# Optimization experiments

Measured on AMD Instinct MI355X. Metric: run time of the kernel, lower is better.

## Reference

```python
import jax, jax.numpy as jnp
import numpy as np

B, L, D = 4, 4096, 1024
H = 16
DK = D // H  # 64
EPS = 1e-5


def setup_inputs() -> dict:
    key = jax.random.key(0)
    ks = jax.random.split(key, 9)
    s = 1.0 / np.sqrt(D)
    return {
        "Q": jax.random.normal(ks[0], (B, L, D), dtype=jnp.float32),
        "W_Q": jax.random.uniform(ks[1], (D, D), jnp.float32, -s, s),
        "b_Q": jax.random.uniform(ks[2], (D,), jnp.float32, -s, s),
        "W_K": jax.random.uniform(ks[3], (D, D), jnp.float32, -s, s),
        "b_K": jax.random.uniform(ks[4], (D,), jnp.float32, -s, s),
        "W_V": jax.random.uniform(ks[5], (D, D), jnp.float32, -s, s),
        "b_V": jax.random.uniform(ks[6], (D,), jnp.float32, -s, s),
        "W_O": jax.random.uniform(ks[7], (D, D), jnp.float32, -s, s),
        "b_O": jax.random.uniform(ks[8], (D,), jnp.float32, -s, s),
    }


def reference(Q, W_Q, b_Q, W_K, b_K, W_V, b_V, W_O, b_O):
    # Projections (torch Linear: x @ W.T + b). K = V = Q (self-attention).
    q = (Q @ W_Q.T + b_Q).reshape(B, L, H, DK)  # blhd
    k = (Q @ W_K.T + b_K).reshape(B, L, H, DK)
    v = (Q @ W_V.T + b_V).reshape(B, L, H, DK)

    phi_q = jax.nn.elu(q) + 1.0
    phi_k = jax.nn.elu(k) + 1.0

    # KV outer-product accumulation over sequence: [b,h,d,m]
    KV = jnp.einsum('blhd,blhm->bhdm', phi_k, v)
    K_sum = phi_k.sum(axis=1)                       # [b,h,d]
    Z = 1.0 / (jnp.einsum('blhd,bhd->blh', phi_q, K_sum) + EPS)
    V_new = jnp.einsum('blhd,bhdm->blhm', phi_q, KV) * Z[..., None]

    out = V_new.reshape(B, L, H * DK) @ W_O.T + b_O  # [b,L,d_model]
    return out
```

## Files before the change

### kernel.cpp

```cpp
#include <hip/hip_runtime.h>

typedef unsigned short u16;
typedef unsigned int   u32;
typedef __attribute__((ext_vector_type(8))) short short8;
typedef __attribute__((ext_vector_type(4))) float f32x4;
typedef __attribute__((ext_vector_type(4))) u16   u16x4;

#define NB 4
#define SL 4096
#define DM 1024
#define NH 16
#define DK 64

__device__ __forceinline__ u16 f2bf(float f) {
  u32 u = __builtin_bit_cast(u32, f);
  u = (u + 0x7fffu + ((u >> 16) & 1u)) >> 16;
  return (u16)u;
}
__device__ __forceinline__ float bf2f(u16 v) {
  u32 u = ((u32)v) << 16;
  return __builtin_bit_cast(float, u);
}
__device__ __forceinline__ float eluP1(float x) {
  return x > 0.f ? x + 1.f : __expf(x);
}
__device__ __forceinline__ void gll16(const u16* g, u16* l) {
  __builtin_amdgcn_global_load_lds((const __attribute__((address_space(1))) void*)g,
                                   (__attribute__((address_space(3))) void*)l, 16, 0, 0);
}

__global__ void cvt_f32_bf16(const float* __restrict__ in, u16* __restrict__ out, int n4) {
  int i = blockIdx.x * 256 + threadIdx.x;
  if (i < n4) {
    f32x4 f = *(const f32x4*)(in + (size_t)i * 4);
    u16x4 o = { f2bf(f[0]), f2bf(f[1]), f2bf(f[2]), f2bf(f[3]) };
    *(u16x4*)(out + (size_t)i * 4) = o;
  }
}

__global__ void cvt_w(const float* __restrict__ WQ, const float* __restrict__ WK,
                      const float* __restrict__ WV, const float* __restrict__ WO,
                      u16* __restrict__ Wqkv, u16* __restrict__ Wobf) {
  int r = blockIdx.x >> 10;
  int i = (blockIdx.x & 1023) * 256 + threadIdx.x;
  const float* src = r == 0 ? WQ : r == 1 ? WK : r == 2 ? WV : WO;
  u16* dst = (r == 3) ? Wobf : Wqkv + (size_t)r * 1048576;
  f32x4 f = *(const f32x4*)(src + (size_t)i * 4);
  u16x4 o = { f2bf(f[0]), f2bf(f[1]), f2bf(f[2]), f2bf(f[3]) };
  *(u16x4*)(dst + (size_t)i * 4) = o;
}

__global__ void pack_bias(const float* __restrict__ bQ, const float* __restrict__ bK,
                          const float* __restrict__ bV, float* __restrict__ biasQKV) {
  int i = blockIdx.x * 256 + threadIdx.x;
  float v = (i < 1024) ? bQ[i] : (i < 2048) ? bK[i - 1024] : bV[i - 2048];
  biasQKV[i] = v;
}

__global__ __launch_bounds__(256) void gemm_qkv(const u16* __restrict__ A,
                                                const u16* __restrict__ Wqkv,
                                                const float* __restrict__ biasQKV,
                                                u16* __restrict__ phiq,
                                                u16* __restrict__ phiKT,
                                                u16* __restrict__ vT) {
  const int K = 1024;
  const int bId = blockIdx.x;
  const int xcd = bId & 7, s = bId >> 3;
  const int tile_n = s >> 4;
  const int tile_m = xcd * 16 + (s & 15);
  const int region = tile_n >> 3;

  const int tid = threadIdx.x, lane = tid & 63, wv = tid >> 6;
  const int i16 = lane & 15, q = lane >> 4;
  const int waveR = wv >> 1, waveC = wv & 1;

  __shared__ u16 smem[17408];

  const int rbase = wv * 32 + (lane >> 2);
  const int kc = (lane & 3) ^ ((rbase >> 1) & 3);
  const u16* Ag = A + (size_t)(tile_m * 128 + rbase) * K + kc * 8;
  const u16* Wg = Wqkv + (size_t)(tile_n * 128 + rbase) * K + kc * 8;

  f32x4 acc[4][4] = {};

  {
    u16* XsB = smem + wv * 1024;
    u16* WsB = smem + 4096 + wv * 1024;
    gll16(Ag, XsB);
    gll16(Ag + 16 * K, XsB + 512);
    gll16(Wg, WsB);
    gll16(Wg + 16 * K, WsB + 512);
  }

  for (int k = 0; k < 32; k++) {
    const int cur = k & 1;
    __syncthreads();
    if (k < 31) {
      const int nxt = cur ^ 1;
      const int k0 = (k + 1) * 32;
      u16* XsB = smem + nxt * 8192 + wv * 1024;
      u16* WsB = smem + nxt * 8192 + 4096 + wv * 1024;
      gll16(Ag + k0,          XsB);
      gll16(Ag + k0 + 16 * K, XsB + 512);
      gll16(Wg + k0,          WsB);
      gll16(Wg + k0 + 16 * K, WsB + 512);
    }
    const u16* Xc = smem + cur * 8192;
    const u16* Wc = Xc + 4096;
    const u16* aT = (region == 0) ? Wc : Xc;
    const u16* bT = (region == 0) ? Xc : Wc;

    short8 af[4], bfr[4];
#pragma unroll
    for (int t = 0; t < 4; t++) {
      int m = waveR * 64 + t * 16 + i16;
      af[t] = *(const short8*)(aT + m * 32 + ((q ^ ((m >> 1) & 3)) << 3));
    }
#pragma unroll
    for (int u = 0; u < 4; u++) {
      int m = waveC * 64 + u * 16 + i16;
      bfr[u] = *(const short8*)(bT + m * 32 + ((q ^ ((m >> 1) & 3)) << 3));
    }
#pragma unroll
    for (int t = 0; t < 4; t++)
#pragma unroll
      for (int u = 0; u < 4; u++)
        acc[t][u] = __builtin_amdgcn_mfma_f32_16x16x32_bf16(af[t], bfr[u], acc[t][u], 0, 0, 0);
  }

  __syncthreads();
  u16* T = smem;
#pragma unroll
  for (int t = 0; t < 4; t++) {
#pragma unroll
    for (int u = 0; u < 4; u++) {
      int cI = waveC * 64 + u * 16 + i16;
      int rI = waveR * 64 + t * 16 + q * 4;
      u16x4 o;
      if (region == 0) {
        f32x4 b4 = *(const f32x4*)(biasQKV + tile_n * 128 + rI);
#pragma unroll
        for (int r = 0; r < 4; r++) o[r] = f2bf(eluP1(acc[t][u][r] + b4[r]));
      } else {
        float bs = biasQKV[tile_n * 128 + cI];
#pragma unroll
        for (int r = 0; r < 4; r++) {
          float vv = acc[t][u][r] + bs;
          if (region == 1) vv = eluP1(vv);
          o[r] = f2bf(vv);
        }
      }
      *(u16x4*)(T + cI * 136 + rI) = o;
    }
  }
  __syncthreads();
  {
    const int Rl = tid >> 4, j = tid & 15;
    u16* dst = (region == 1) ? phiKT : vT;
#pragma unroll
    for (int p = 0; p < 8; p++) {
      int R = p * 16 + Rl;
      short8 v8 = *(const short8*)(T + R * 136 + j * 8);
      if (region == 0) {
        *(short8*)(phiq + (size_t)(tile_m * 128 + R) * DM + tile_n * 128 + j * 8) = v8;
      } else {
        int n_loc = tile_n * 128 + R - region * 1024;
        int bI = tile_m >> 5;
        int l = (tile_m & 31) * 128 + j * 8;
        *(short8*)(dst + ((size_t)bI * 1024 + n_loc) * 4096 + l) = v8;
      }
    }
  }
}

__global__ __launch_bounds__(256) void gemm_out(const u16* __restrict__ A,
                                                const u16* __restrict__ W,
                                                const float* __restrict__ bias,
                                                float* __restrict__ outp) {
  const int K = 1024;
  const int bId = blockIdx.x;
  const int xcd = bId & 7, s = bId >> 3;
  const int tile_n = s >> 4;
  const int tile_m = xcd * 16 + (s & 15);

  const int tid = threadIdx.x, lane = tid & 63, wv = tid >> 6;
  const int i16 = lane & 15, q = lane >> 4;
  const int waveR = wv >> 1, waveC = wv & 1;

  __shared__ u16 smem[17408];

  const int rbase = wv * 32 + (lane >> 2);
  const int kc = (lane & 3) ^ ((rbase >> 1) & 3);
  const u16* Ag = A + (size_t)(tile_m * 128 + rbase) * K + kc * 8;
  const u16* Wg = W + (size_t)(tile_n * 128 + rbase) * K + kc * 8;

  f32x4 acc[4][4] = {};

  {
    u16* XsB = smem + wv * 1024;
    u16* WsB = smem + 4096 + wv * 1024;
    gll16(Ag, XsB);
    gll16(Ag + 16 * K, XsB + 512);
    gll16(Wg, WsB);
    gll16(Wg + 16 * K, WsB + 512);
  }

  for (int k = 0; k < 32; k++) {
    const int cur = k & 1;
    __syncthreads();
    if (k < 31) {
      const int nxt = cur ^ 1;
      const int k0 = (k + 1) * 32;
      u16* XsB = smem + nxt * 8192 + wv * 1024;
      u16* WsB = smem + nxt * 8192 + 4096 + wv * 1024;
      gll16(Ag + k0,          XsB);
      gll16(Ag + k0 + 16 * K, XsB + 512);
      gll16(Wg + k0,          WsB);
      gll16(Wg + k0 + 16 * K, WsB + 512);
    }
    const u16* Xc = smem + cur * 8192;
    const u16* Wc = Xc + 4096;

    short8 af[4], bfr[4];
#pragma unroll
    for (int t = 0; t < 4; t++) {
      int m = waveR * 64 + t * 16 + i16;
      af[t] = *(const short8*)(Wc + m * 32 + ((q ^ ((m >> 1) & 3)) << 3));
    }
#pragma unroll
    for (int u = 0; u < 4; u++) {
      int m = waveC * 64 + u * 16 + i16;
      bfr[u] = *(const short8*)(Xc + m * 32 + ((q ^ ((m >> 1) & 3)) << 3));
    }
#pragma unroll
    for (int t = 0; t < 4; t++)
#pragma unroll
      for (int u = 0; u < 4; u++)
        acc[t][u] = __builtin_amdgcn_mfma_f32_16x16x32_bf16(af[t], bfr[u], acc[t][u], 0, 0, 0);
  }

  float* Tf = (float*)smem;
#pragma unroll
  for (int half = 0; half < 2; half++) {
    __syncthreads();
    if (waveR == half) {
#pragma unroll
      for (int t = 0; t < 4; t++) {
#pragma unroll
        for (int u = 0; u < 4; u++) {
          int cI = waveC * 64 + u * 16 + i16;
          int rIh = t * 16 + q * 4;
          f32x4 b4 = *(const f32x4*)(bias + tile_n * 128 + half * 64 + rIh);
          f32x4 o;
#pragma unroll
          for (int r = 0; r < 4; r++) o[r] = acc[t][u][r] + b4[r];
          *(f32x4*)(Tf + cI * 68 + rIh) = o;
        }
      }
    }
    __syncthreads();
    const int Rl = tid >> 4, j = tid & 15;
#pragma unroll
    for (int p = 0; p < 8; p++) {
      int R = p * 16 + Rl;
      f32x4 v = *(const f32x4*)(Tf + R * 68 + j * 4);
      *(f32x4*)(outp + (size_t)(tile_m * 128 + R) * DM + tile_n * 128 + half * 64 + j * 4) = v;
    }
  }
}

__global__ __launch_bounds__(256) void kv_partial(const u16* __restrict__ phiKT,
                                                  const u16* __restrict__ vT,
                                                  float* __restrict__ part,
                                                  float* __restrict__ ksumP) {
  int bh = blockIdx.x >> 2, chunk = blockIdx.x & 3;
  int tid = threadIdx.x, lane = tid & 63, wv = tid >> 6;
  int i16 = lane & 15, q = lane >> 4;
  const u16* Ab = phiKT + (size_t)bh * DK * SL;
  const u16* Bb = vT + (size_t)bh * DK * SL;
  int l0 = (chunk * 4 + wv) * 256;
  f32x4 acc[4][4] = {};
  float ks[4] = {};
  for (int kk = 0; kk < 256; kk += 32) {
    int col = l0 + kk + q * 8;
    short8 af[4], bfr[4];
#pragma unroll
    for (int t = 0; t < 4; t++) af[t] = *(const short8*)(Ab + (size_t)(t * 16 + i16) * SL + col);
#pragma unroll
    for (int u = 0; u < 4; u++) bfr[u] = *(const short8*)(Bb + (size_t)(u * 16 + i16) * SL + col);
#pragma unroll
    for (int t = 0; t < 4; t++)
#pragma unroll
      for (int j = 0; j < 8; j++) ks[t] += bf2f((u16)af[t][j]);
#pragma unroll
    for (int t = 0; t < 4; t++)
#pragma unroll
      for (int u = 0; u < 4; u++)
        acc[t][u] = __builtin_amdgcn_mfma_f32_16x16x32_bf16(af[t], bfr[u], acc[t][u], 0, 0, 0);
  }
  __shared__ float red[4][64][64];
  __shared__ float ksl[4][4][64];
#pragma unroll
  for (int t = 0; t < 4; t++)
#pragma unroll
    for (int u = 0; u < 4; u++)
#pragma unroll
      for (int r = 0; r < 4; r++)
        red[wv][t * 16 + q * 4 + r][u * 16 + i16] = acc[t][u][r];
#pragma unroll
  for (int t = 0; t < 4; t++) ksl[wv][q][t * 16 + i16] = ks[t];
  __syncthreads();
  int d = tid >> 2, mg = (tid & 3) * 16;
#pragma unroll
  for (int c = 0; c < 4; c++) {
    int m = mg + c * 4;
    f32x4 o;
#pragma unroll
    for (int r = 0; r < 4; r++)
      o[r] = red[0][d][m + r] + red[1][d][m + r] + red[2][d][m + r] + red[3][d][m + r];
    *(f32x4*)(part + ((size_t)(chunk * 64 + bh) * 64 + d) * 64 + m) = o;
  }
  if (tid < 64) {
    float s = 0.f;
#pragma unroll
    for (int w2 = 0; w2 < 4; w2++)
#pragma unroll
      for (int q2 = 0; q2 < 4; q2++) s += ksl[w2][q2][tid];
    ksumP[chunk * 4096 + bh * 64 + tid] = s;
  }
}

__global__ __launch_bounds__(256) void kv_finalize(const float* __restrict__ part,
                                                   const float* __restrict__ ksumP,
                                                   u16* __restrict__ KVt,
                                                   float* __restrict__ Ksum) {
  int bh = blockIdx.x, tid = threadIdx.x;
  for (int e = tid; e < 4096; e += 256) {
    int d = e >> 6, m = e & 63;
    float s = part[((size_t)(0 * 64 + bh) * 64 + d) * 64 + m]
            + part[((size_t)(1 * 64 + bh) * 64 + d) * 64 + m]
            + part[((size_t)(2 * 64 + bh) * 64 + d) * 64 + m]
            + part[((size_t)(3 * 64 + bh) * 64 + d) * 64 + m];
    KVt[(size_t)bh * 4096 + m * 64 + d] = f2bf(s);
  }
  if (tid < 64) {
    float s = ksumP[0 * 4096 + bh * 64 + tid] + ksumP[1 * 4096 + bh * 64 + tid]
            + ksumP[2 * 4096 + bh * 64 + tid] + ksumP[3 * 4096 + bh * 64 + tid];
    Ksum[bh * 64 + tid] = s;
  }
}

__global__ __launch_bounds__(256) void vnew_kernel(const u16* __restrict__ phiq,
                                                   const u16* __restrict__ KVt,
                                                   const float* __restrict__ Ksum,
                                                   u16* __restrict__ Vnew) {
  int bh = blockIdx.x >> 5, lt = blockIdx.x & 31;
  int b = bh >> 4, h = bh & 15;
  int tid = threadIdx.x, lane = tid & 63, wv = tid >> 6;
  int i16 = lane & 15, q = lane >> 4;
  int waveM = wv & 1, waveL = wv >> 1;

  __shared__ float Zs[128];
  __shared__ float Pp[128][2];
  __shared__ u16 T[128 * 72];
  {
    int l = tid >> 1, half = tid & 1;
    const u16* pr = phiq + (size_t)(b * SL + lt * 128 + l) * DM + h * 64 + half * 32;
    float s = 0.f;
    for (int i = 0; i < 32; i += 8) {
      short8 v8 = *(const short8*)(pr + i);
#pragma unroll
      for (int j = 0; j < 8; j++) s += bf2f((u16)v8[j]) * Ksum[bh * 64 + half * 32 + i + j];
    }
    Pp[l][half] = s;
  }
  __syncthreads();
  if (tid < 128) Zs[tid] = 1.0f / (Pp[tid][0] + Pp[tid][1] + 1e-5f);
  __syncthreads();

  f32x4 acc[2][4] = {};
#pragma unroll
  for (int step = 0; step < 2; step++) {
    int d0 = step * 32 + q * 8;
    short8 af[2], bfr[4];
#pragma unroll
    for (int t = 0; t < 2; t++) {
      int m = waveM * 32 + t * 16 + i16;
      af[t] = *(const short8*)(KVt + (size_t)bh * 4096 + m * 64 + d0);
    }
#pragma unroll
    for (int u = 0; u < 4; u++) {
      int l = lt * 128 + waveL * 64 + u * 16 + i16;
      bfr[u] = *(const short8*)(phiq + (size_t)(b * SL + l) * DM + h * 64 + d0);
    }
#pragma unroll
    for (int t = 0; t < 2; t++)
#pragma unroll
      for (int u = 0; u < 4; u++)
        acc[t][u] = __builtin_amdgcn_mfma_f32_16x16x32_bf16(af[t], bfr[u], acc[t][u], 0, 0, 0);
  }

#pragma unroll
  for (int t = 0; t < 2; t++) {
#pragma unroll
    for (int u = 0; u < 4; u++) {
      int cI = waveL * 64 + u * 16 + i16;
      int nI = waveM * 32 + t * 16 + q * 4;
      float z = Zs[cI];
      u16x4 o;
#pragma unroll
      for (int r = 0; r < 4; r++) o[r] = f2bf(acc[t][u][r] * z);
      *(u16x4*)(T + cI * 72 + nI) = o;
    }
  }
  __syncthreads();
  {
    const int Rl = tid >> 3, j = tid & 7;
#pragma unroll
    for (int p = 0; p < 4; p++) {
      int R = p * 32 + Rl;
      short8 v8 = *(const short8*)(T + R * 72 + j * 8);
      *(short8*)(Vnew + (size_t)(b * SL + lt * 128 + R) * DM + h * 64 + j * 8) = v8;
    }
  }
}

extern "C" void kernel_launch(void* const* d_in, const int* in_sizes, int n_in,
                              void* d_out, int out_size, void* d_ws, size_t ws_size,
                              hipStream_t stream) {
  const float* Qf = (const float*)d_in[0];
  const float* WQ = (const float*)d_in[1];
  const float* bQ = (const float*)d_in[2];
  const float* WK = (const float*)d_in[3];
  const float* bK = (const float*)d_in[4];
  const float* WV = (const float*)d_in[5];
  const float* bV = (const float*)d_in[6];
  const float* WO = (const float*)d_in[7];
  const float* bO = (const float*)d_in[8];

  const size_t MB = 1024ull * 1024ull;
  char* ws = (char*)d_ws;
  u16* Qbf     = (u16*)(ws + 0);
  u16* Vnew    = (u16*)(ws + 0);
  u16* Wqkv    = (u16*)(ws + 32 * MB);
  u16* Wobf    = (u16*)(ws + 38 * MB);
  float* biasQKV = (float*)(ws + 40 * MB);
  u16* phiq    = (u16*)(ws + 41 * MB);
  u16* phiKT   = (u16*)(ws + 73 * MB);
  u16* vT      = (u16*)(ws + 105 * MB);
  u16* KVt     = (u16*)(ws + 137 * MB);
  float* Ksum  = (float*)(ws + 138 * MB);
  float* part  = (float*)(ws + 139 * MB);
  float* ksumP = (float*)(ws + 143 * MB);

  cvt_f32_bf16<<<16384, 256, 0, stream>>>(Qf, Qbf, 4194304);
  cvt_w<<<4096, 256, 0, stream>>>(WQ, WK, WV, WO, Wqkv, Wobf);
  pack_bias<<<12, 256, 0, stream>>>(bQ, bK, bV, biasQKV);

  gemm_qkv<<<3072, 256, 0, stream>>>(Qbf, Wqkv, biasQKV, phiq, phiKT, vT);

  kv_partial<<<256, 256, 0, stream>>>(phiKT, vT, part, ksumP);
  kv_finalize<<<64, 256, 0, stream>>>(part, ksumP, KVt, Ksum);

  vnew_kernel<<<2048, 256, 0, stream>>>(phiq, KVt, Ksum, Vnew);

  gemm_out<<<1024, 256, 0, stream>>>(Vnew, Wobf, bO, (float*)d_out);
}
```

Baseline: 372.4 us.

## Fuse conversion kernels, remap GEMM tiles per XCD, unroll K loop with precomputed LDS pointers

Merges the three input conversion kernels into one launch to cut launch overhead. Both GEMMs remap block indices so each XCD covers a 2D patch of tiles (32x12 or 32x4) for better L2 reuse of A and W. The K loop is unrolled by two with ping-pong buffers and precomputed LDS fragment pointers, which removes per-iteration address arithmetic and branch logic. The QKV epilogue now stages the tile in two halves through a smaller LDS buffer, which adds extra barriers.

```diff
diff --git a/kernel.cpp b/kernel.cpp
--- a/kernel.cpp
+++ b/kernel.cpp
@@ -24,38 +24,59 @@
 __device__ __forceinline__ float eluP1(float x) {
   return x > 0.f ? x + 1.f : __expf(x);
 }
-__device__ __forceinline__ void gll16(const u16* g, u16* l) {
-  __builtin_amdgcn_global_load_lds((const __attribute__((address_space(1))) void*)g,
-                                   (__attribute__((address_space(3))) void*)l, 16, 0, 0);
-}
-
-__global__ void cvt_f32_bf16(const float* __restrict__ in, u16* __restrict__ out, int n4) {
-  int i = blockIdx.x * 256 + threadIdx.x;
-  if (i < n4) {
-    f32x4 f = *(const f32x4*)(in + (size_t)i * 4);
+#define GLL(gp, lp) __builtin_amdgcn_global_load_lds(     \
+    (const __attribute__((address_space(1))) void*)(gp),  \
+    (__attribute__((address_space(3))) void*)(lp), 16, 0, 0)
+
+__global__ void cvt_all(const float* __restrict__ Qf,
+                        const float* __restrict__ WQ, const float* __restrict__ WK,
+                        const float* __restrict__ WV, const float* __restrict__ WO,
+                        const float* __restrict__ bQ, const float* __restrict__ bK,
+                        const float* __restrict__ bV,
+                        u16* __restrict__ Qbf, u16* __restrict__ Wqkv,
+                        u16* __restrict__ Wobf, float* __restrict__ biasQKV) {
+  int b = blockIdx.x, tid = threadIdx.x;
+  if (b < 16384) {
+    int i = b * 256 + tid;
+    f32x4 f = *(const f32x4*)(Qf + (size_t)i * 4);
     u16x4 o = { f2bf(f[0]), f2bf(f[1]), f2bf(f[2]), f2bf(f[3]) };
-    *(u16x4*)(out + (size_t)i * 4) = o;
-  }
-}
-
-__global__ void cvt_w(const float* __restrict__ WQ, const float* __restrict__ WK,
-                      const float* __restrict__ WV, const float* __restrict__ WO,
-                      u16* __restrict__ Wqkv, u16* __restrict__ Wobf) {
-  int r = blockIdx.x >> 10;
-  int i = (blockIdx.x & 1023) * 256 + threadIdx.x;
-  const float* src = r == 0 ? WQ : r == 1 ? WK : r == 2 ? WV : WO;
-  u16* dst = (r == 3) ? Wobf : Wqkv + (size_t)r * 1048576;
-  f32x4 f = *(const f32x4*)(src + (size_t)i * 4);
-  u16x4 o = { f2bf(f[0]), f2bf(f[1]), f2bf(f[2]), f2bf(f[3]) };
-  *(u16x4*)(dst + (size_t)i * 4) = o;
-}
-
-__global__ void pack_bias(const float* __restrict__ bQ, const float* __restrict__ bK,
-                          const float* __restrict__ bV, float* __restrict__ biasQKV) {
-  int i = blockIdx.x * 256 + threadIdx.x;
-  float v = (i < 1024) ? bQ[i] : (i < 2048) ? bK[i - 1024] : bV[i - 2048];
-  biasQKV[i] = v;
-}
+    *(u16x4*)(Qbf + (size_t)i * 4) = o;
+  } else if (b < 20480) {
+    int r = (b - 16384) >> 10;
+    int i = ((b - 16384) & 1023) * 256 + tid;
+    const float* src = r == 0 ? WQ : r == 1 ? WK : r == 2 ? WV : WO;
+    u16* dst = (r == 3) ? Wobf : Wqkv + (size_t)r * 1048576;
+    f32x4 f = *(const f32x4*)(src + (size_t)i * 4);
+    u16x4 o = { f2bf(f[0]), f2bf(f[1]), f2bf(f[2]), f2bf(f[3]) };
+    *(u16x4*)(dst + (size_t)i * 4) = o;
+  } else {
+    int i = (b - 20480) * 256 + tid;
+    if (i < 3072) {
+      float v = (i < 1024) ? bQ[i] : (i < 2048) ? bK[i - 1024] : bV[i - 2048];
+      biasQKV[i] = v;
+    }
+  }
+}
+
+#define COMPUTE(CB)                                                          \
+  do {                                                                       \
+    short8 af_[4], bf_[4];                                                   \
+    _Pragma("unroll") for (int t = 0; t < 4; t++)                            \
+        af_[t] = *(const short8*)(aP[t] + (CB));                             \
+    _Pragma("unroll") for (int u = 0; u < 4; u++)                            \
+        bf_[u] = *(const short8*)(bP[u] + (CB));                             \
+    _Pragma("unroll") for (int t = 0; t < 4; t++)                            \
+      _Pragma("unroll") for (int u = 0; u < 4; u++)                          \
+          acc[t][u] = __builtin_amdgcn_mfma_f32_16x16x32_bf16(               \
+              af_[t], bf_[u], acc[t][u], 0, 0, 0);                           \
+  } while (0)
+
+#define STAGE4(XB, WB)                                        \
+  do {                                                        \
+    GLL(Ag0, XB); GLL(Ag1, (XB) + 512);                       \
+    GLL(Wg0, WB); GLL(Wg1, (WB) + 512);                       \
+    Ag0 += 32; Ag1 += 32; Wg0 += 32; Wg1 += 32;               \
+  } while (0)
 
 __global__ __launch_bounds__(256) void gemm_qkv(const u16* __restrict__ A,
                                                 const u16* __restrict__ Wqkv,
@@ -66,108 +87,100 @@
   const int K = 1024;
   const int bId = blockIdx.x;
   const int xcd = bId & 7, s = bId >> 3;
-  const int tile_n = s >> 4;
-  const int tile_m = xcd * 16 + (s & 15);
+  const int xm = xcd >> 1, xn = xcd & 1;
+  const int tm_l = s / 12, tn_l = s - tm_l * 12;
+  const int tile_m = xm * 32 + tm_l;
+  const int tile_n = xn * 12 + tn_l;
   const int region = tile_n >> 3;
 
   const int tid = threadIdx.x, lane = tid & 63, wv = tid >> 6;
   const int i16 = lane & 15, q = lane >> 4;
   const int waveR = wv >> 1, waveC = wv & 1;
 
-  __shared__ u16 smem[17408];
+  __shared__ u16 smem[16384];
 
   const int rbase = wv * 32 + (lane >> 2);
   const int kc = (lane & 3) ^ ((rbase >> 1) & 3);
-  const u16* Ag = A + (size_t)(tile_m * 128 + rbase) * K + kc * 8;
-  const u16* Wg = Wqkv + (size_t)(tile_n * 128 + rbase) * K + kc * 8;
+  const u16* Ag0 = A + (size_t)(tile_m * 128 + rbase) * K + kc * 8;
+  const u16* Ag1 = Ag0 + 16 * K;
+  const u16* Wg0 = Wqkv + (size_t)(tile_n * 128 + rbase) * K + kc * 8;
+  const u16* Wg1 = Wg0 + 16 * K;
+  u16* X0 = smem + wv * 1024;
+  u16* W0 = smem + 4096 + wv * 1024;
+  u16* X1 = X0 + 8192;
+  u16* W1 = W0 + 8192;
+
+  const u16* aT0 = (region == 0) ? smem + 4096 : smem;
+  const u16* bT0 = (region == 0) ? smem : smem + 4096;
+  const u16* aP[4];
+  const u16* bP[4];
+#pragma unroll
+  for (int t = 0; t < 4; t++) {
+    int m = waveR * 64 + t * 16 + i16;
+    aP[t] = aT0 + m * 32 + ((q ^ ((m >> 1) & 3)) << 3);
+  }
+#pragma unroll
+  for (int u = 0; u < 4; u++) {
+    int m = waveC * 64 + u * 16 + i16;
+    bP[u] = bT0 + m * 32 + ((q ^ ((m >> 1) & 3)) << 3);
+  }
 
   f32x4 acc[4][4] = {};
 
-  {
-    u16* XsB = smem + wv * 1024;
-    u16* WsB = smem + 4096 + wv * 1024;
-    gll16(Ag, XsB);
-    gll16(Ag + 16 * K, XsB + 512);
-    gll16(Wg, WsB);
-    gll16(Wg + 16 * K, WsB + 512);
-  }
-
-  for (int k = 0; k < 32; k++) {
-    const int cur = k & 1;
-    __syncthreads();
-    if (k < 31) {
-      const int nxt = cur ^ 1;
-      const int k0 = (k + 1) * 32;
-      u16* XsB = smem + nxt * 8192 + wv * 1024;
-      u16* WsB = smem + nxt * 8192 + 4096 + wv * 1024;
-      gll16(Ag + k0,          XsB);
-      gll16(Ag + k0 + 16 * K, XsB + 512);
-      gll16(Wg + k0,          WsB);
-      gll16(Wg + k0 + 16 * K, WsB + 512);
-    }
-    const u16* Xc = smem + cur * 8192;
-    const u16* Wc = Xc + 4096;
-    const u16* aT = (region == 0) ? Wc : Xc;
-    const u16* bT = (region == 0) ? Xc : Wc;
-
-    short8 af[4], bfr[4];
-#pragma unroll
-    for (int t = 0; t < 4; t++) {
-      int m = waveR * 64 + t * 16 + i16;
-      af[t] = *(const short8*)(aT + m * 32 + ((q ^ ((m >> 1) & 3)) << 3));
-    }
-#pragma unroll
-    for (int u = 0; u < 4; u++) {
-      int m = waveC * 64 + u * 16 + i16;
-      bfr[u] = *(const short8*)(bT + m * 32 + ((q ^ ((m >> 1) & 3)) << 3));
-    }
-#pragma unroll
-    for (int t = 0; t < 4; t++)
-#pragma unroll
-      for (int u = 0; u < 4; u++)
-        acc[t][u] = __builtin_amdgcn_mfma_f32_16x16x32_bf16(af[t], bfr[u], acc[t][u], 0, 0, 0);
-  }
-
-  __syncthreads();
+  STAGE4(X0, W0);
+
+  for (int kk = 0; kk < 16; kk++) {
+    __syncthreads();
+    STAGE4(X1, W1);
+    COMPUTE(0);
+    __syncthreads();
+    if (kk < 15) STAGE4(X0, W0);
+    COMPUTE(8192);
+  }
+
   u16* T = smem;
-#pragma unroll
-  for (int t = 0; t < 4; t++) {
-#pragma unroll
-    for (int u = 0; u < 4; u++) {
-      int cI = waveC * 64 + u * 16 + i16;
-      int rI = waveR * 64 + t * 16 + q * 4;
-      u16x4 o;
-      if (region == 0) {
-        f32x4 b4 = *(const f32x4*)(biasQKV + tile_n * 128 + rI);
-#pragma unroll
-        for (int r = 0; r < 4; r++) o[r] = f2bf(eluP1(acc[t][u][r] + b4[r]));
-      } else {
-        float bs = biasQKV[tile_n * 128 + cI];
-#pragma unroll
-        for (int r = 0; r < 4; r++) {
-          float vv = acc[t][u][r] + bs;
-          if (region == 1) vv = eluP1(vv);
-          o[r] = f2bf(vv);
+  u16* dstT = (region == 1) ? phiKT : vT;
+#pragma unroll
+  for (int h = 0; h < 2; h++) {
+    __syncthreads();
+    if (waveR == h) {
+#pragma unroll
+      for (int t = 0; t < 4; t++) {
+#pragma unroll
+        for (int u = 0; u < 4; u++) {
+          int cI = waveC * 64 + u * 16 + i16;
+          int rI = t * 16 + q * 4;
+          u16x4 o;
+          if (region == 0) {
+            f32x4 b4 = *(const f32x4*)(biasQKV + tile_n * 128 + h * 64 + rI);
+#pragma unroll
+            for (int r = 0; r < 4; r++) o[r] = f2bf(eluP1(acc[t][u][r] + b4[r]));
+          } else {
+            float bs = biasQKV[tile_n * 128 + cI];
+#pragma unroll
+            for (int r = 0; r < 4; r++) {
+              float vv = acc[t][u][r] + bs;
+              if (region == 1) vv = eluP1(vv);
+              o[r] = f2bf(vv);
+            }
+          }
+          *(u16x4*)(T + cI * 72 + rI) = o;
         }
       }
-      *(u16x4*)(T + cI * 136 + rI) = o;
-    }
-  }
-  __syncthreads();
-  {
-    const int Rl = tid >> 4, j = tid & 15;
-    u16* dst = (region == 1) ? phiKT : vT;
-#pragma unroll
-    for (int p = 0; p < 8; p++) {
-      int R = p * 16 + Rl;
-      short8 v8 = *(const short8*)(T + R * 136 + j * 8);
+    }
+    __syncthreads();
+    const int Rl = tid >> 3, j = tid & 7;
+#pragma unroll
+    for (int p = 0; p < 4; p++) {
+      int R = p * 32 + Rl;
+      short8 v8 = *(const short8*)(T + R * 72 + j * 8);
       if (region == 0) {
-        *(short8*)(phiq + (size_t)(tile_m * 128 + R) * DM + tile_n * 128 + j * 8) = v8;
+        *(short8*)(phiq + (size_t)(tile_m * 128 + R) * DM + tile_n * 128 + h * 64 + j * 8) = v8;
       } else {
         int n_loc = tile_n * 128 + R - region * 1024;
         int bI = tile_m >> 5;
-        int l = (tile_m & 31) * 128 + j * 8;
-        *(short8*)(dst + ((size_t)bI * 1024 + n_loc) * 4096 + l) = v8;
+        int l = (tile_m & 31) * 128 + h * 64 + j * 8;
+        *(short8*)(dstT + ((size_t)bI * 1024 + n_loc) * 4096 + l) = v8;
       }
     }
   }
@@ -180,8 +193,10 @@
   const int K = 1024;
   const int bId = blockIdx.x;
   const int xcd = bId & 7, s = bId >> 3;
-  const int tile_n = s >> 4;
-  const int tile_m = xcd * 16 + (s & 15);
+  const int xm = xcd >> 1, xn = xcd & 1;
+  const int tm_l = s >> 2, tn_l = s & 3;
+  const int tile_m = xm * 32 + tm_l;
+  const int tile_n = xn * 4 + tn_l;
 
   const int tid = threadIdx.x, lane = tid & 63, wv = tid >> 6;
   const int i16 = lane & 15, q = lane >> 4;
@@ -191,52 +206,39 @@
 
   const int rbase = wv * 32 + (lane >> 2);
   const int kc = (lane & 3) ^ ((rbase >> 1) & 3);
-  const u16* Ag = A + (size_t)(tile_m * 128 + rbase) * K + kc * 8;
-  const u16* Wg = W + (size_t)(tile_n * 128 + rbase) * K + kc * 8;
+  const u16* Ag0 = A + (size_t)(tile_m * 128 + rbase) * K + kc * 8;
+  const u16* Ag1 = Ag0 + 16 * K;
+  const u16* Wg0 = W + (size_t)(tile_n * 128 + rbase) * K + kc * 8;
+  const u16* Wg1 = Wg0 + 16 * K;
+  u16* X0 = smem + wv * 1024;
+  u16* W0 = smem + 4096 + wv * 1024;
+  u16* X1 = X0 + 8192;
+  u16* W1 = W0 + 8192;
+
+  const u16* aP[4];
+  const u16* bP[4];
+#pragma unroll
+  for (int t = 0; t < 4; t++) {
+    int m = waveR * 64 + t * 16 + i16;
+    aP[t] = smem + 4096 + m * 32 + ((q ^ ((m >> 1) & 3)) << 3);
+  }
+#pragma unroll
+  for (int u = 0; u < 4; u++) {
+    int m = waveC * 64 + u * 16 + i16;
+    bP[u] = smem + m * 32 + ((q ^ ((m >> 1) & 3)) << 3);
+  }
 
   f32x4 acc[4][4] = {};
 
-  {
-    u16* XsB = smem + wv * 1024;
-    u16* WsB = smem + 4096 + wv * 1024;
-    gll16(Ag, XsB);
-    gll16(Ag + 16 * K, XsB + 512);
-    gll16(Wg, WsB);
-    gll16(Wg + 16 * K, WsB + 512);
-  }
-
-  for (int k = 0; k < 32; k++) {
-    const int cur = k & 1;
-    __syncthreads();
-    if (k < 31) {
-      const int nxt = cur ^ 1;
-      const int k0 = (k + 1) * 32;
-      u16* XsB = smem + nxt * 8192 + wv * 1024;
-      u16* WsB = smem + nxt * 8192 + 4096 + wv * 1024;
-      gll16(Ag + k0,          XsB);
-      gll16(Ag + k0 + 16 * K, XsB + 512);
-      gll16(Wg + k0,          WsB);
-      gll16(Wg + k0 + 16 * K, WsB + 512);
-    }
-    const u16* Xc = smem + cur * 8192;
-    const u16* Wc = Xc + 4096;
-
-    short8 af[4], bfr[4];
-#pragma unroll
-    for (int t = 0; t < 4; t++) {
-      int m = waveR * 64 + t * 16 + i16;
-      af[t] = *(const short8*)(Wc + m * 32 + ((q ^ ((m >> 1) & 3)) << 3));
-    }
-#pragma unroll
-    for (int u = 0; u < 4; u++) {
-      int m = waveC * 64 + u * 16 + i16;
-      bfr[u] = *(const short8*)(Xc + m * 32 + ((q ^ ((m >> 1) & 3)) << 3));
-    }
-#pragma unroll
-    for (int t = 0; t < 4; t++)
-#pragma unroll
-      for (int u = 0; u < 4; u++)
-        acc[t][u] = __builtin_amdgcn_mfma_f32_16x16x32_bf16(af[t], bfr[u], acc[t][u], 0, 0, 0);
+  STAGE4(X0, W0);
+
+  for (int kk = 0; kk < 16; kk++) {
+    __syncthreads();
+    STAGE4(X1, W1);
+    COMPUTE(0);
+    __syncthreads();
+    if (kk < 15) STAGE4(X0, W0);
+    COMPUTE(8192);
   }
 
   float* Tf = (float*)smem;
@@ -453,9 +455,8 @@
   float* part  = (float*)(ws + 139 * MB);
   float* ksumP = (float*)(ws + 143 * MB);
 
-  cvt_f32_bf16<<<16384, 256, 0, stream>>>(Qf, Qbf, 4194304);
-  cvt_w<<<4096, 256, 0, stream>>>(WQ, WK, WV, WO, Wqkv, Wobf);
-  pack_bias<<<12, 256, 0, stream>>>(bQ, bK, bV, biasQKV);
+  cvt_all<<<20492, 256, 0, stream>>>(Qf, WQ, WK, WV, WO, bQ, bK, bV,
+                                     Qbf, Wqkv, Wobf, biasQKV);
 
   gemm_qkv<<<3072, 256, 0, stream>>>(Qbf, Wqkv, biasQKV, phiq, phiKT, vT);
 
```

Result: faster. 361.4 us (-2.9%).
